# Kernel optimization log

Hardware: AMD Instinct MI355X
Metric: run time of the kernel (lower is better)

## Reference

```python
import jax, jax.numpy as jnp
import numpy as np

STATE_DIM = 128
N_RBF = 20
R_CUT = 10.0
N_NODES = 25000
N_EDGES = 250000
N_GRAPHS = 512
N_ATOMS = 100
NUM_ROUNDS = 1


def setup_inputs() -> dict:
    key = jax.random.key(0)
    ks = jax.random.split(key, 20)
    D = STATE_DIM

    def w(k, shape, s=0.05):
        return jax.random.normal(k, shape, jnp.float32) * s

    return {
        "edge_vec": jax.random.normal(ks[0], (N_EDGES, 3), jnp.float32),
        "embedding": w(ks[1], (N_ATOMS, D), 1.0),
        "phi_W1": w(ks[2], (D, D)), "phi_b1": jnp.zeros((D,), jnp.float32),
        "phi_W2": w(ks[3], (D, 3 * D)), "phi_b2": jnp.zeros((3 * D,), jnp.float32),
        "filt_W": w(ks[4], (N_RBF, 3 * D)), "filt_b": jnp.zeros((3 * D,), jnp.float32),
        "upd_W1": w(ks[5], (2 * D, D)), "upd_b1": jnp.zeros((D,), jnp.float32),
        "upd_W2": w(ks[6], (D, 3 * D)), "upd_b2": jnp.zeros((3 * D,), jnp.float32),
        "out_W1": w(ks[7], (D, D)), "out_b1": jnp.zeros((D,), jnp.float32),
        "out_W2": w(ks[8], (D, 1)), "out_b2": jnp.zeros((1,), jnp.float32),
        "U_W": w(ks[9], (D, D)),
        "V_W": w(ks[10], (D, D)),
        "atom_types": jax.random.randint(ks[11], (N_NODES,), 0, N_ATOMS),
        "node_from": jax.random.randint(ks[12], (N_EDGES,), 0, N_NODES),
        "node_to": jax.random.randint(ks[13], (N_EDGES,), 0, N_NODES),
        "node_graph_index": jnp.sort(jax.random.randint(ks[14], (N_NODES,), 0, N_GRAPHS)),
        "num_graphs": N_GRAPHS,
    }


def _painn_forward(edge_vec, embedding, phi_W1, phi_b1, phi_W2, phi_b2,
                   filt_W, filt_b, upd_W1, upd_b1, upd_W2, upd_b2,
                   out_W1, out_b1, out_W2, out_b2, U_W, V_W,
                   atom_types, node_from, node_to, node_graph_index, num_graphs):
    silu = jax.nn.silu
    D = STATE_DIM
    # initial node scalar states from atom-type embedding; vector states zero
    state = embedding[atom_types]                         # [N, D]
    state_vec = jnp.zeros((state.shape[0], 3, D), state.dtype)  # [N, 3, D]

    # edge geometry (constant across rounds)
    d = jnp.linalg.norm(edge_vec, axis=1, keepdims=True)  # [E, 1]
    kfreq = jnp.arange(1, N_RBF + 1, dtype=jnp.float32)   # PaiNN sinc radial basis
    rbf = jnp.sin(kfreq * jnp.pi * d / R_CUT) / d         # [E, n]
    fc = 0.5 * (jnp.cos(jnp.pi * d / R_CUT) + 1.0) * (d < R_CUT)  # cosine cutoff [E,1]
    W_out = (rbf @ filt_W + filt_b) * fc                  # [E, 3D]
    normalized = edge_vec / d                             # [E, 3]

    for _ in range(NUM_ROUNDS):
        # --- message block ---
        inp = state[node_from]                             # gather [E, D]
        phi = silu(inp @ phi_W1 + phi_b1) @ phi_W2 + phi_b2  # [E, 3D]
        pf = phi * W_out                                   # [E, 3D]
        m1, m2, m3 = pf[:, :D], pf[:, D:2 * D], pf[:, 2 * D:]
        msg_vec = (state_vec[node_from] * m1[:, None, :]
                   + normalized[:, :, None] * m3[:, None, :])  # [E, 3, D]
        state = state.at[node_to].add(m2)                  # scatter-add scalars
        state_vec = state_vec.at[node_to].add(msg_vec)     # scatter-add vectors

        # --- update block (torch detaches state_vec here) ---
        sv = jax.lax.stop_gradient(state_vec)
        Up = sv @ U_W                                      # [N, 3, D]
        Vp = sv @ V_W                                      # [N, 3, D]
        UV = jnp.sum(Up * Vp, axis=1)                      # [N, D]
        Vn = jnp.linalg.norm(Vp, axis=1)                   # [N, D]
        h = jnp.concatenate([Vn, state], axis=1)           # [N, 2D]
        a = silu(h @ upd_W1 + upd_b1) @ upd_W2 + upd_b2    # [N, 3D]
        a_vv, a_sv, a_ss = a[:, :D], a[:, D:2 * D], a[:, 2 * D:]
        state = state + a_ss + UV * a_sv
        state_vec = state_vec + Up * a_vv[:, None, :]

    idx = node_graph_index - node_graph_index[0]
    graph_state = jax.ops.segment_sum(state, idx, num_segments=num_graphs)  # [G, D]
    return silu(graph_state @ out_W1 + out_b1) @ out_W2 + out_b2            # [G, 1]


def reference(edge_vec, embedding, phi_W1, phi_b1, phi_W2, phi_b2,
              filt_W, filt_b, upd_W1, upd_b1, upd_W2, upd_b2,
              out_W1, out_b1, out_W2, out_b2, U_W, V_W,
              atom_types, node_from, node_to, node_graph_index, num_graphs):
    return _painn_forward(edge_vec, embedding, phi_W1, phi_b1, phi_W2, phi_b2,
                          filt_W, filt_b, upd_W1, upd_b1, upd_W2, upd_b2,
                          out_W1, out_b1, out_W2, out_b2, U_W, V_W,
                          atom_types, node_from, node_to, node_graph_index, num_graphs)
```

## Files before the change

### kernel.cpp

```cpp
#include <hip/hip_runtime.h>
#include <math.h>

#define D 128
#define NRBF 20
#define NEDGES 250000
#define NNODES 25000
#define NGRAPHS 512
#define NATOMS 100

constexpr float RCUT = 10.0f;
constexpr float PI_F = 3.14159265358979323846f;

__device__ __forceinline__ float silu_f(float x) { return x / (1.0f + __expf(-x)); }

__global__ __launch_bounds__(128) void k_phi_table(
    const float* __restrict__ emb, const float* __restrict__ W1, const float* __restrict__ b1,
    const float* __restrict__ W2, const float* __restrict__ b2, float* __restrict__ phi_tab)
{
    __shared__ float s_in[D];
    __shared__ float s_hid[D];
    const int t = blockIdx.x;
    const int j = threadIdx.x;
    s_in[j] = emb[t * D + j];
    __syncthreads();
    float acc = b1[j];
    for (int c = 0; c < D; ++c) acc = fmaf(s_in[c], W1[c * D + j], acc);
    s_hid[j] = silu_f(acc);
    __syncthreads();
    #pragma unroll
    for (int r = 0; r < 3; ++r) {
        const int col = r * D + j;
        float a2 = b2[col];
        for (int c = 0; c < D; ++c) a2 = fmaf(s_hid[c], W2[c * 384 + col], a2);
        phi_tab[t * 384 + col] = a2;
    }
}

__global__ void k_zero(int* __restrict__ counts, float* __restrict__ gs)
{
    const int i = blockIdx.x * 256 + threadIdx.x;
    if (i < NNODES) counts[i] = 0;
    if (i < NGRAPHS * D) gs[i] = 0.f;
}

__global__ void k_hist(const int* __restrict__ node_to, int* __restrict__ counts)
{
    const int e = blockIdx.x * 256 + threadIdx.x;
    if (e < NEDGES) atomicAdd(&counts[node_to[e]], 1);
}

__global__ __launch_bounds__(1024) void k_scan(int* __restrict__ counts,
                                               int* __restrict__ row_ptr)
{
    __shared__ int s[1024];
    const int t = threadIdx.x;
    const int base = t * 25;
    int sum = 0;
    for (int j = 0; j < 25; ++j) {
        const int idx = base + j;
        if (idx < NNODES) sum += counts[idx];
    }
    s[t] = sum;
    __syncthreads();
    for (int off = 1; off < 1024; off <<= 1) {
        int v = 0;
        if (t >= off) v = s[t - off];
        __syncthreads();
        if (t >= off) s[t] += v;
        __syncthreads();
    }
    int run = (t > 0) ? s[t - 1] : 0;
    for (int j = 0; j < 25; ++j) {
        const int idx = base + j;
        if (idx < NNODES) {
            const int v = counts[idx];
            row_ptr[idx] = run;
            counts[idx] = run;
            run += v;
        }
    }
    if (t == 1023) row_ptr[NNODES] = s[1023];
}

__global__ __launch_bounds__(256) void k_pre(
    const float* __restrict__ edge_vec, const int* __restrict__ node_from,
    const int* __restrict__ node_to, const int* __restrict__ atom_types,
    int* __restrict__ cursor, float* __restrict__ edata, int* __restrict__ ety)
{
    const int e = blockIdx.x * 256 + threadIdx.x;
    if (e >= NEDGES) return;
    const float x = edge_vec[e * 3 + 0];
    const float y = edge_vec[e * 3 + 1];
    const float z = edge_vec[e * 3 + 2];
    const float d = sqrtf(x * x + y * y + z * z);
    const float inv = 1.0f / d;
    const float th = PI_F * d / RCUT;
    const float fc = (d < RCUT) ? 0.5f * (__cosf(th) + 1.0f) : 0.0f;
    const float sc = fc * inv;

    float buf[24];
    #pragma unroll
    for (int k = 0; k < NRBF; ++k) buf[k] = __sinf((float)(k + 1) * th) * sc;
    buf[20] = fc;
    buf[21] = x * inv;
    buf[22] = y * inv;
    buf[23] = z * inv;

    const int slot = atomicAdd(&cursor[node_to[e]], 1);
    float* o = edata + (size_t)slot * 24;
    #pragma unroll
    for (int q = 0; q < 6; ++q) *(float4*)(o + q * 4) = *(float4*)&buf[q * 4];
    ety[slot] = atom_types[node_from[e]];
}

#define GNPB 8
__global__ __launch_bounds__(128) void k_gather(
    const int* __restrict__ row_ptr, const float* __restrict__ edata,
    const int* __restrict__ ety, const float* __restrict__ phi_tab,
    const float* __restrict__ filt_W, const float* __restrict__ filt_b,
    const float* __restrict__ emb, const int* __restrict__ atom_types,
    float* __restrict__ state, float* __restrict__ sv)
{
    const int t = threadIdx.x;
    const int c1 = 128 + t;
    const int c2 = 256 + t;
    float fw1[NRBF], fw2[NRBF];
    #pragma unroll
    for (int k = 0; k < NRBF; ++k) {
        fw1[k] = filt_W[k * 384 + c1];
        fw2[k] = filt_W[k * 384 + c2];
    }
    const float fb1 = filt_b[c1];
    const float fb2 = filt_b[c2];

    #pragma unroll 1
    for (int ni = 0; ni < GNPB; ++ni) {
        const int n = blockIdx.x * GNPB + ni;
        const int r0 = row_ptr[n];
        const int r1 = row_ptr[n + 1];
        float as0 = 0.f, av0 = 0.f, av1 = 0.f, av2 = 0.f;
        for (int i = r0; i < r1; ++i) {
            const float4* p = (const float4*)(edata + (size_t)i * 24);
            const float4 q0 = p[0], q1 = p[1], q2 = p[2], q3 = p[3], q4 = p[4], q5 = p[5];
            const int ty = ety[i];
            float w1 = fb1 * q5.x, w2 = fb2 * q5.x;
            w1 = fmaf(q0.x, fw1[0], w1);  w2 = fmaf(q0.x, fw2[0], w2);
            w1 = fmaf(q0.y, fw1[1], w1);  w2 = fmaf(q0.y, fw2[1], w2);
            w1 = fmaf(q0.z, fw1[2], w1);  w2 = fmaf(q0.z, fw2[2], w2);
            w1 = fmaf(q0.w, fw1[3], w1);  w2 = fmaf(q0.w, fw2[3], w2);
            w1 = fmaf(q1.x, fw1[4], w1);  w2 = fmaf(q1.x, fw2[4], w2);
            w1 = fmaf(q1.y, fw1[5], w1);  w2 = fmaf(q1.y, fw2[5], w2);
            w1 = fmaf(q1.z, fw1[6], w1);  w2 = fmaf(q1.z, fw2[6], w2);
            w1 = fmaf(q1.w, fw1[7], w1);  w2 = fmaf(q1.w, fw2[7], w2);
            w1 = fmaf(q2.x, fw1[8], w1);  w2 = fmaf(q2.x, fw2[8], w2);
            w1 = fmaf(q2.y, fw1[9], w1);  w2 = fmaf(q2.y, fw2[9], w2);
            w1 = fmaf(q2.z, fw1[10], w1); w2 = fmaf(q2.z, fw2[10], w2);
            w1 = fmaf(q2.w, fw1[11], w1); w2 = fmaf(q2.w, fw2[11], w2);
            w1 = fmaf(q3.x, fw1[12], w1); w2 = fmaf(q3.x, fw2[12], w2);
            w1 = fmaf(q3.y, fw1[13], w1); w2 = fmaf(q3.y, fw2[13], w2);
            w1 = fmaf(q3.z, fw1[14], w1); w2 = fmaf(q3.z, fw2[14], w2);
            w1 = fmaf(q3.w, fw1[15], w1); w2 = fmaf(q3.w, fw2[15], w2);
            w1 = fmaf(q4.x, fw1[16], w1); w2 = fmaf(q4.x, fw2[16], w2);
            w1 = fmaf(q4.y, fw1[17], w1); w2 = fmaf(q4.y, fw2[17], w2);
            w1 = fmaf(q4.z, fw1[18], w1); w2 = fmaf(q4.z, fw2[18], w2);
            w1 = fmaf(q4.w, fw1[19], w1); w2 = fmaf(q4.w, fw2[19], w2);
            const float pf1 = phi_tab[ty * 384 + c1] * w1;
            const float pf2 = phi_tab[ty * 384 + c2] * w2;
            as0 += pf1;
            av0 = fmaf(q5.y, pf2, av0);
            av1 = fmaf(q5.z, pf2, av1);
            av2 = fmaf(q5.w, pf2, av2);
        }
        state[n * D + t] = emb[atom_types[n] * D + t] + as0;
        float* b = sv + (size_t)n * 3 * D + t;
        b[0]   = av0;
        b[128] = av1;
        b[256] = av2;
    }
}

#define BNUV 16
__global__ __launch_bounds__(256) void k_uv(
    const float* __restrict__ sv, const float* __restrict__ U_W, const float* __restrict__ V_W,
    float* __restrict__ UVb, float* __restrict__ Vnb)
{
    __shared__ __align__(16) float s_sv[BNUV][3][36];
    __shared__ __align__(16) float s_u[32][128];
    __shared__ __align__(16) float s_v[32][128];
    const int t = threadIdx.x;
    const int cg = t & 15;
    const int ni = t >> 4;
    const int node0 = blockIdx.x * BNUV;

    float up[3][8], vp[3][8];
    #pragma unroll
    for (int a = 0; a < 3; ++a)
        #pragma unroll
        for (int h = 0; h < 8; ++h) { up[a][h] = 0.f; vp[a][h] = 0.f; }

    for (int kt = 0; kt < 4; ++kt) {
        __syncthreads();
        for (int i = t; i < 1024; i += 256) {
            const int row = i >> 5, col = (i & 31) * 4;
            *(float4*)&s_u[row][col] = *(const float4*)(U_W + (kt * 32 + row) * 128 + col);
            *(float4*)&s_v[row][col] = *(const float4*)(V_W + (kt * 32 + row) * 128 + col);
        }
        for (int i = t; i < 384; i += 256) {
            const int nd = i / 24;
            const int rem = i - nd * 24;
            const int a = rem >> 3, c4 = (rem & 7) * 4;
            float4 v = make_float4(0.f, 0.f, 0.f, 0.f);
            if (node0 + nd < NNODES)
                v = *(const float4*)(sv + (size_t)(node0 + nd) * 384 + a * 128 + kt * 32 + c4);
            *(float4*)&s_sv[nd][a][c4] = v;
        }
        __syncthreads();
        #pragma unroll 8
        for (int k = 0; k < 32; ++k) {
            const float xs0 = s_sv[ni][0][k];
            const float xs1 = s_sv[ni][1][k];
            const float xs2 = s_sv[ni][2][k];
            const float4 ua = *(const float4*)&s_u[k][cg * 4];
            const float4 ub = *(const float4*)&s_u[k][64 + cg * 4];
            const float4 va = *(const float4*)&s_v[k][cg * 4];
            const float4 vb = *(const float4*)&s_v[k][64 + cg * 4];
            #define UVSTEP(a, XV) \
                up[a][0] = fmaf(XV, ua.x, up[a][0]); up[a][1] = fmaf(XV, ua.y, up[a][1]); \
                up[a][2] = fmaf(XV, ua.z, up[a][2]); up[a][3] = fmaf(XV, ua.w, up[a][3]); \
                up[a][4] = fmaf(XV, ub.x, up[a][4]); up[a][5] = fmaf(XV, ub.y, up[a][5]); \
                up[a][6] = fmaf(XV, ub.z, up[a][6]); up[a][7] = fmaf(XV, ub.w, up[a][7]); \
                vp[a][0] = fmaf(XV, va.x, vp[a][0]); vp[a][1] = fmaf(XV, va.y, vp[a][1]); \
                vp[a][2] = fmaf(XV, va.z, vp[a][2]); vp[a][3] = fmaf(XV, va.w, vp[a][3]); \
                vp[a][4] = fmaf(XV, vb.x, vp[a][4]); vp[a][5] = fmaf(XV, vb.y, vp[a][5]); \
                vp[a][6] = fmaf(XV, vb.z, vp[a][6]); vp[a][7] = fmaf(XV, vb.w, vp[a][7]);
            UVSTEP(0, xs0) UVSTEP(1, xs1) UVSTEP(2, xs2)
            #undef UVSTEP
        }
    }

    const int n = node0 + ni;
    if (n < NNODES) {
        float uvr[8], vnr[8];
        #pragma unroll
        for (int h = 0; h < 8; ++h) {
            uvr[h] = up[0][h] * vp[0][h] + up[1][h] * vp[1][h] + up[2][h] * vp[2][h];
            vnr[h] = sqrtf(vp[0][h] * vp[0][h] + vp[1][h] * vp[1][h] + vp[2][h] * vp[2][h]);
        }
        float* uo = UVb + n * D;
        float* vo = Vnb + n * D;
        *(float4*)(uo + cg * 4)      = *(float4*)&uvr[0];
        *(float4*)(uo + 64 + cg * 4) = *(float4*)&uvr[4];
        *(float4*)(vo + cg * 4)      = *(float4*)&vnr[0];
        *(float4*)(vo + 64 + cg * 4) = *(float4*)&vnr[4];
    }
}

#define BN1 64
__global__ __launch_bounds__(256) void k_mlp1(
    const float* __restrict__ Vnb, const float* __restrict__ state,
    const float* __restrict__ W1, const float* __restrict__ b1,
    float* __restrict__ hid)
{
    __shared__ __align__(16) float s_h[BN1][36];
    __shared__ __align__(16) float s_w[32][128];
    const int t = threadIdx.x;
    const int cg = t & 15;
    const int rg = t >> 4;
    const int n0 = blockIdx.x * BN1;

    float acc[4][8];
    #pragma unroll
    for (int r = 0; r < 4; ++r)
        #pragma unroll
        for (int h = 0; h < 8; ++h)
            acc[r][h] = (h < 4) ? b1[cg * 4 + h] : b1[64 + cg * 4 + (h - 4)];

    for (int kt = 0; kt < 8; ++kt) {
        const float* src = (kt < 4) ? (Vnb + kt * 32) : (state + (kt - 4) * 32);
        __syncthreads();
        #pragma unroll
        for (int q = 0; q < 2; ++q) {
            const int i = t * 2 + q;
            const int row = i >> 3, c4 = (i & 7) * 4;
            float4 v = make_float4(0.f, 0.f, 0.f, 0.f);
            if (n0 + row < NNODES) v = *(const float4*)(src + (size_t)(n0 + row) * D + c4);
            *(float4*)&s_h[row][c4] = v;
        }
        #pragma unroll
        for (int q = 0; q < 4; ++q) {
            const int i = t + q * 256;
            const int row = i >> 5, col = (i & 31) * 4;
            *(float4*)&s_w[row][col] = *(const float4*)(W1 + (kt * 32 + row) * 128 + col);
        }
        __syncthreads();
        #pragma unroll 8
        for (int k = 0; k < 32; ++k) {
            const float4 wa = *(const float4*)&s_w[k][cg * 4];
            const float4 wb = *(const float4*)&s_w[k][64 + cg * 4];
            #pragma unroll
            for (int r = 0; r < 4; ++r) {
                const float x = s_h[rg * 4 + r][k];
                acc[r][0] = fmaf(x, wa.x, acc[r][0]); acc[r][1] = fmaf(x, wa.y, acc[r][1]);
                acc[r][2] = fmaf(x, wa.z, acc[r][2]); acc[r][3] = fmaf(x, wa.w, acc[r][3]);
                acc[r][4] = fmaf(x, wb.x, acc[r][4]); acc[r][5] = fmaf(x, wb.y, acc[r][5]);
                acc[r][6] = fmaf(x, wb.z, acc[r][6]); acc[r][7] = fmaf(x, wb.w, acc[r][7]);
            }
        }
    }

    #pragma unroll
    for (int r = 0; r < 4; ++r) {
        const int n = n0 + rg * 4 + r;
        if (n < NNODES) {
            float lo[4], hi[4];
            #pragma unroll
            for (int h = 0; h < 4; ++h) { lo[h] = silu_f(acc[r][h]); hi[h] = silu_f(acc[r][h + 4]); }
            *(float4*)(hid + (size_t)n * D + cg * 4)      = *(float4*)lo;
            *(float4*)(hid + (size_t)n * D + 64 + cg * 4) = *(float4*)hi;
        }
    }
}

#define BN2 64
__global__ __launch_bounds__(256) void k_mlp2(
    const float* __restrict__ hid, const float* __restrict__ state,
    const float* __restrict__ UVb,
    const float* __restrict__ W2, const float* __restrict__ b2,
    const int* __restrict__ ngi, float* __restrict__ gs)
{
    __shared__ __align__(16) float s_h[BN2][36];
    __shared__ __align__(16) float s_w2[32][256];
    const int t = threadIdx.x;
    const int cg = t & 15;
    const int rg = t >> 4;
    const int n0 = blockIdx.x * BN2;

    float acc[4][16];
    #pragma unroll
    for (int r = 0; r < 4; ++r)
        #pragma unroll
        for (int g = 0; g < 4; ++g)
            #pragma unroll
            for (int h = 0; h < 4; ++h)
                acc[r][g * 4 + h] = b2[128 + g * 64 + cg * 4 + h];

    for (int kt = 0; kt < 4; ++kt) {
        __syncthreads();
        #pragma unroll
        for (int q = 0; q < 2; ++q) {
            const int i = t * 2 + q;
            const int row = i >> 3, c4 = (i & 7) * 4;
            float4 v = make_float4(0.f, 0.f, 0.f, 0.f);
            if (n0 + row < NNODES)
                v = *(const float4*)(hid + (size_t)(n0 + row) * D + kt * 32 + c4);
            *(float4*)&s_h[row][c4] = v;
        }
        #pragma unroll
        for (int q = 0; q < 8; ++q) {
            const int i = t + q * 256;
            const int row = i >> 6, col = (i & 63) * 4;
            *(float4*)&s_w2[row][col] = *(const float4*)(W2 + (kt * 32 + row) * 384 + 128 + col);
        }
        __syncthreads();
        #pragma unroll 4
        for (int k = 0; k < 32; ++k) {
            const float4 w0 = *(const float4*)&s_w2[k][cg * 4];
            const float4 w1 = *(const float4*)&s_w2[k][64 + cg * 4];
            const float4 w2v = *(const float4*)&s_w2[k][128 + cg * 4];
            const float4 w3 = *(const float4*)&s_w2[k][192 + cg * 4];
            #pragma unroll
            for (int r = 0; r < 4; ++r) {
                const float x = s_h[rg * 4 + r][k];
                acc[r][0]  = fmaf(x, w0.x, acc[r][0]);  acc[r][1]  = fmaf(x, w0.y, acc[r][1]);
                acc[r][2]  = fmaf(x, w0.z, acc[r][2]);  acc[r][3]  = fmaf(x, w0.w, acc[r][3]);
                acc[r][4]  = fmaf(x, w1.x, acc[r][4]);  acc[r][5]  = fmaf(x, w1.y, acc[r][5]);
                acc[r][6]  = fmaf(x, w1.z, acc[r][6]);  acc[r][7]  = fmaf(x, w1.w, acc[r][7]);
                acc[r][8]  = fmaf(x, w2v.x, acc[r][8]); acc[r][9]  = fmaf(x, w2v.y, acc[r][9]);
                acc[r][10] = fmaf(x, w2v.z, acc[r][10]);acc[r][11] = fmaf(x, w2v.w, acc[r][11]);
                acc[r][12] = fmaf(x, w3.x, acc[r][12]); acc[r][13] = fmaf(x, w3.y, acc[r][13]);
                acc[r][14] = fmaf(x, w3.z, acc[r][14]); acc[r][15] = fmaf(x, w3.w, acc[r][15]);
            }
        }
    }

    const int g0 = ngi[0];
    int gprev = -1;
    float run[8];
    #pragma unroll
    for (int r = 0; r < 4; ++r) {
        const int n = n0 + rg * 4 + r;
        if (n >= NNODES) break;
        const int g = ngi[n] - g0;
        const float4 stA = *(const float4*)(state + (size_t)n * D + cg * 4);
        const float4 stB = *(const float4*)(state + (size_t)n * D + 64 + cg * 4);
        const float4 uvA = *(const float4*)(UVb + (size_t)n * D + cg * 4);
        const float4 uvB = *(const float4*)(UVb + (size_t)n * D + 64 + cg * 4);
        float val[8];
        val[0] = stA.x + acc[r][8]  + uvA.x * acc[r][0];
        val[1] = stA.y + acc[r][9]  + uvA.y * acc[r][1];
        val[2] = stA.z + acc[r][10] + uvA.z * acc[r][2];
        val[3] = stA.w + acc[r][11] + uvA.w * acc[r][3];
        val[4] = stB.x + acc[r][12] + uvB.x * acc[r][4];
        val[5] = stB.y + acc[r][13] + uvB.y * acc[r][5];
        val[6] = stB.z + acc[r][14] + uvB.z * acc[r][6];
        val[7] = stB.w + acc[r][15] + uvB.w * acc[r][7];
        if (g == gprev) {
            #pragma unroll
            for (int h = 0; h < 8; ++h) run[h] += val[h];
        } else {
            if (gprev >= 0) {
                float* grow = gs + (size_t)gprev * D;
                #pragma unroll
                for (int h = 0; h < 4; ++h) unsafeAtomicAdd(grow + cg * 4 + h, run[h]);
                #pragma unroll
                for (int h = 0; h < 4; ++h) unsafeAtomicAdd(grow + 64 + cg * 4 + h, run[h + 4]);
            }
            #pragma unroll
            for (int h = 0; h < 8; ++h) run[h] = val[h];
            gprev = g;
        }
    }
    if (gprev >= 0) {
        float* grow = gs + (size_t)gprev * D;
        #pragma unroll
        for (int h = 0; h < 4; ++h) unsafeAtomicAdd(grow + cg * 4 + h, run[h]);
        #pragma unroll
        for (int h = 0; h < 4; ++h) unsafeAtomicAdd(grow + 64 + cg * 4 + h, run[h + 4]);
    }
}

__global__ __launch_bounds__(128) void k_out(
    const float* __restrict__ gs, const float* __restrict__ W1, const float* __restrict__ b1,
    const float* __restrict__ W2, const float* __restrict__ b2, float* __restrict__ out)
{
    __shared__ float s_g[D];
    __shared__ float s_part[2];
    const int g = blockIdx.x;
    const int j = threadIdx.x;
    s_g[j] = gs[g * D + j];
    __syncthreads();
    float acc = b1[j];
    for (int c = 0; c < D; ++c) acc = fmaf(s_g[c], W1[c * D + j], acc);
    float m = silu_f(acc) * W2[j];
    #pragma unroll
    for (int off = 32; off > 0; off >>= 1) m += __shfl_down(m, off);
    if ((j & 63) == 0) s_part[j >> 6] = m;
    __syncthreads();
    if (j == 0) out[g] = s_part[0] + s_part[1] + b2[0];
}

extern "C" void kernel_launch(void* const* d_in, const int* in_sizes, int n_in,
                              void* d_out, int out_size, void* d_ws, size_t ws_size,
                              hipStream_t stream) {
    const float* edge_vec  = (const float*)d_in[0];
    const float* embedding = (const float*)d_in[1];
    const float* phi_W1    = (const float*)d_in[2];
    const float* phi_b1    = (const float*)d_in[3];
    const float* phi_W2    = (const float*)d_in[4];
    const float* phi_b2    = (const float*)d_in[5];
    const float* filt_W    = (const float*)d_in[6];
    const float* filt_b    = (const float*)d_in[7];
    const float* upd_W1    = (const float*)d_in[8];
    const float* upd_b1    = (const float*)d_in[9];
    const float* upd_W2    = (const float*)d_in[10];
    const float* upd_b2    = (const float*)d_in[11];
    const float* out_W1    = (const float*)d_in[12];
    const float* out_b1    = (const float*)d_in[13];
    const float* out_W2    = (const float*)d_in[14];
    const float* out_b2    = (const float*)d_in[15];
    const float* U_W       = (const float*)d_in[16];
    const float* V_W       = (const float*)d_in[17];
    const int* atom_types  = (const int*)d_in[18];
    const int* node_from   = (const int*)d_in[19];
    const int* node_to     = (const int*)d_in[20];
    const int* ngi         = (const int*)d_in[21];
    float* out = (float*)d_out;

    float* ws = (float*)d_ws;
    float* phi_tab = ws;
    float* state   = phi_tab + NATOMS * 384;
    float* sv      = state + NNODES * D;
    float* gsb     = sv + (size_t)NNODES * 3 * D;
    float* scratch = gsb + NGRAPHS * D;
    int*   row_ptr = (int*)scratch;
    int*   counts  = row_ptr + NNODES + 1;
    int*   ety     = counts + NNODES;
    float* edata   = scratch + 300004;
    float* UVb     = scratch;
    float* Vnb     = scratch + NNODES * D;
    float* hid     = sv;

    k_phi_table<<<NATOMS, 128, 0, stream>>>(embedding, phi_W1, phi_b1, phi_W2, phi_b2, phi_tab);
    k_zero<<<(NGRAPHS * D + 255) / 256, 256, 0, stream>>>(counts, gsb);
    k_hist<<<(NEDGES + 255) / 256, 256, 0, stream>>>(node_to, counts);
    k_scan<<<1, 1024, 0, stream>>>(counts, row_ptr);
    k_pre<<<(NEDGES + 255) / 256, 256, 0, stream>>>(
        edge_vec, node_from, node_to, atom_types, counts, edata, ety);
    k_gather<<<NNODES / GNPB, 128, 0, stream>>>(
        row_ptr, edata, ety, phi_tab, filt_W, filt_b, embedding, atom_types, state, sv);
    k_uv<<<(NNODES + BNUV - 1) / BNUV, 256, 0, stream>>>(sv, U_W, V_W, UVb, Vnb);
    k_mlp1<<<(NNODES + BN1 - 1) / BN1, 256, 0, stream>>>(Vnb, state, upd_W1, upd_b1, hid);
    k_mlp2<<<(NNODES + BN2 - 1) / BN2, 256, 0, stream>>>(hid, state, UVb, upd_W2, upd_b2, ngi, gsb);
    k_out<<<NGRAPHS, 128, 0, stream>>>(gsb, out_W1, out_b1, out_W2, out_b2, out);
}
```

Baseline: 423.0 us.

## Stage edge data in shared memory and split gather channels across thread halves

The gather kernel now processes 16 nodes per 256-thread block. It cooperatively loads chunks of 64 edges' radial data and source types into shared memory and streams them across node boundaries using the CSR row pointers. Each half of the block computes one filter channel group (scalar or vector), which halves per-thread registers and FMA chains and removes the per-thread redundant global edge loads. The cost is extra block synchronisation and a serial edge walk in which all threads share the same node-boundary handling.

```diff
diff --git a/kernel.cpp b/kernel.cpp
--- a/kernel.cpp
+++ b/kernel.cpp
@@ -113,69 +113,96 @@
     ety[slot] = atom_types[node_from[e]];
 }
 
-#define GNPB 8
-__global__ __launch_bounds__(128) void k_gather(
+#define GNPB 16
+#define CHUNK 64
+__global__ __launch_bounds__(256) void k_gather(
     const int* __restrict__ row_ptr, const float* __restrict__ edata,
     const int* __restrict__ ety, const float* __restrict__ phi_tab,
     const float* __restrict__ filt_W, const float* __restrict__ filt_b,
     const float* __restrict__ emb, const int* __restrict__ atom_types,
     float* __restrict__ state, float* __restrict__ sv)
 {
+    __shared__ __align__(16) float s_ed[CHUNK * 24];
+    __shared__ int s_ep[CHUNK];
+    __shared__ int s_rp[GNPB + 1];
+
     const int t = threadIdx.x;
-    const int c1 = 128 + t;
-    const int c2 = 256 + t;
-    float fw1[NRBF], fw2[NRBF];
-    #pragma unroll
-    for (int k = 0; k < NRBF; ++k) {
-        fw1[k] = filt_W[k * 384 + c1];
-        fw2[k] = filt_W[k * 384 + c2];
-    }
-    const float fb1 = filt_b[c1];
-    const float fb2 = filt_b[c2];
-
-    #pragma unroll 1
-    for (int ni = 0; ni < GNPB; ++ni) {
-        const int n = blockIdx.x * GNPB + ni;
-        const int r0 = row_ptr[n];
-        const int r1 = row_ptr[n + 1];
-        float as0 = 0.f, av0 = 0.f, av1 = 0.f, av2 = 0.f;
-        for (int i = r0; i < r1; ++i) {
-            const float4* p = (const float4*)(edata + (size_t)i * 24);
+    const bool is_m2 = (t < 128);
+    const int lane = is_m2 ? t : (t - 128);
+    const int c = is_m2 ? (128 + lane) : (256 + lane);
+
+    const int n0 = blockIdx.x * GNPB;
+    const int nEnd = min(n0 + GNPB, NNODES);
+
+    if (t <= GNPB) s_rp[t] = row_ptr[min(n0 + t, NNODES)];
+
+    float fw[NRBF];
+    #pragma unroll
+    for (int k = 0; k < NRBF; ++k) fw[k] = filt_W[k * 384 + c];
+    const float fb = filt_b[c];
+
+    __syncthreads();
+    const int e0 = s_rp[0];
+    const int e1 = s_rp[nEnd - n0];
+
+    int cur = n0;
+    int nb = s_rp[1];
+    float a0 = 0.f, a1 = 0.f, a2 = 0.f;
+
+    for (int base = e0; base < e1; base += CHUNK) {
+        const int cnt = min(CHUNK, e1 - base);
+        __syncthreads();
+        for (int i = t; i < cnt * 6; i += 256)
+            ((float4*)s_ed)[i] = ((const float4*)edata)[(size_t)base * 6 + i];
+        for (int i = t; i < cnt; i += 256) s_ep[i] = ety[base + i];
+        __syncthreads();
+
+        for (int j = 0; j < cnt; ++j) {
+            const int g = base + j;
+            while (g >= nb) {
+                if (is_m2) {
+                    state[cur * D + lane] = emb[atom_types[cur] * D + lane] + a0;
+                } else {
+                    float* b = sv + (size_t)cur * 3 * D + lane;
+                    b[0] = a0; b[128] = a1; b[256] = a2;
+                }
+                a0 = a1 = a2 = 0.f;
+                ++cur;
+                nb = s_rp[cur - n0 + 1];
+            }
+            const float4* p = (const float4*)(s_ed + j * 24);
             const float4 q0 = p[0], q1 = p[1], q2 = p[2], q3 = p[3], q4 = p[4], q5 = p[5];
-            const int ty = ety[i];
-            float w1 = fb1 * q5.x, w2 = fb2 * q5.x;
-            w1 = fmaf(q0.x, fw1[0], w1);  w2 = fmaf(q0.x, fw2[0], w2);
-            w1 = fmaf(q0.y, fw1[1], w1);  w2 = fmaf(q0.y, fw2[1], w2);
-            w1 = fmaf(q0.z, fw1[2], w1);  w2 = fmaf(q0.z, fw2[2], w2);
-            w1 = fmaf(q0.w, fw1[3], w1);  w2 = fmaf(q0.w, fw2[3], w2);
-            w1 = fmaf(q1.x, fw1[4], w1);  w2 = fmaf(q1.x, fw2[4], w2);
-            w1 = fmaf(q1.y, fw1[5], w1);  w2 = fmaf(q1.y, fw2[5], w2);
-            w1 = fmaf(q1.z, fw1[6], w1);  w2 = fmaf(q1.z, fw2[6], w2);
-            w1 = fmaf(q1.w, fw1[7], w1);  w2 = fmaf(q1.w, fw2[7], w2);
-            w1 = fmaf(q2.x, fw1[8], w1);  w2 = fmaf(q2.x, fw2[8], w2);
-            w1 = fmaf(q2.y, fw1[9], w1);  w2 = fmaf(q2.y, fw2[9], w2);
-            w1 = fmaf(q2.z, fw1[10], w1); w2 = fmaf(q2.z, fw2[10], w2);
-            w1 = fmaf(q2.w, fw1[11], w1); w2 = fmaf(q2.w, fw2[11], w2);
-            w1 = fmaf(q3.x, fw1[12], w1); w2 = fmaf(q3.x, fw2[12], w2);
-            w1 = fmaf(q3.y, fw1[13], w1); w2 = fmaf(q3.y, fw2[13], w2);
-            w1 = fmaf(q3.z, fw1[14], w1); w2 = fmaf(q3.z, fw2[14], w2);
-            w1 = fmaf(q3.w, fw1[15], w1); w2 = fmaf(q3.w, fw2[15], w2);
-            w1 = fmaf(q4.x, fw1[16], w1); w2 = fmaf(q4.x, fw2[16], w2);
-            w1 = fmaf(q4.y, fw1[17], w1); w2 = fmaf(q4.y, fw2[17], w2);
-            w1 = fmaf(q4.z, fw1[18], w1); w2 = fmaf(q4.z, fw2[18], w2);
-            w1 = fmaf(q4.w, fw1[19], w1); w2 = fmaf(q4.w, fw2[19], w2);
-            const float pf1 = phi_tab[ty * 384 + c1] * w1;
-            const float pf2 = phi_tab[ty * 384 + c2] * w2;
-            as0 += pf1;
-            av0 = fmaf(q5.y, pf2, av0);
-            av1 = fmaf(q5.z, pf2, av1);
-            av2 = fmaf(q5.w, pf2, av2);
-        }
-        state[n * D + t] = emb[atom_types[n] * D + t] + as0;
-        float* b = sv + (size_t)n * 3 * D + t;
-        b[0]   = av0;
-        b[128] = av1;
-        b[256] = av2;
+            const int ty = s_ep[j];
+            float w = fb * q5.x;
+            w = fmaf(q0.x, fw[0], w);  w = fmaf(q0.y, fw[1], w);
+            w = fmaf(q0.z, fw[2], w);  w = fmaf(q0.w, fw[3], w);
+            w = fmaf(q1.x, fw[4], w);  w = fmaf(q1.y, fw[5], w);
+            w = fmaf(q1.z, fw[6], w);  w = fmaf(q1.w, fw[7], w);
+            w = fmaf(q2.x, fw[8], w);  w = fmaf(q2.y, fw[9], w);
+            w = fmaf(q2.z, fw[10], w); w = fmaf(q2.w, fw[11], w);
+            w = fmaf(q3.x, fw[12], w); w = fmaf(q3.y, fw[13], w);
+            w = fmaf(q3.z, fw[14], w); w = fmaf(q3.w, fw[15], w);
+            w = fmaf(q4.x, fw[16], w); w = fmaf(q4.y, fw[17], w);
+            w = fmaf(q4.z, fw[18], w); w = fmaf(q4.w, fw[19], w);
+            const float pf = phi_tab[ty * 384 + c] * w;
+            if (is_m2) {
+                a0 += pf;
+            } else {
+                a0 = fmaf(q5.y, pf, a0);
+                a1 = fmaf(q5.z, pf, a1);
+                a2 = fmaf(q5.w, pf, a2);
+            }
+        }
+    }
+    while (cur < nEnd) {
+        if (is_m2) {
+            state[cur * D + lane] = emb[atom_types[cur] * D + lane] + a0;
+        } else {
+            float* b = sv + (size_t)cur * 3 * D + lane;
+            b[0] = a0; b[128] = a1; b[256] = a2;
+        }
+        a0 = a1 = a2 = 0.f;
+        ++cur;
     }
 }
 
@@ -496,7 +523,7 @@
     k_scan<<<1, 1024, 0, stream>>>(counts, row_ptr);
     k_pre<<<(NEDGES + 255) / 256, 256, 0, stream>>>(
         edge_vec, node_from, node_to, atom_types, counts, edata, ety);
-    k_gather<<<NNODES / GNPB, 128, 0, stream>>>(
+    k_gather<<<(NNODES + GNPB - 1) / GNPB, 256, 0, stream>>>(
         row_ptr, edata, ety, phi_tab, filt_W, filt_b, embedding, atom_types, state, sv);
     k_uv<<<(NNODES + BNUV - 1) / BNUV, 256, 0, stream>>>(sv, U_W, V_W, UVb, Vnb);
     k_mlp1<<<(NNODES + BN1 - 1) / BN1, 256, 0, stream>>>(Vnb, state, upd_W1, upd_b1, hid);
```

After: 431.3 us. Within noise of the previous version (+2.0%).
